# Kernel optimization log

Measured on AMD Instinct MI355X. Metric: run time of the kernel, lower is better.

The kernel has to match this reference:

```python
import jax, jax.numpy as jnp
import numpy as np
import math

H = 16
D = 1024
DH = D // H  # 64


def setup_inputs() -> dict:
    key = jax.random.key(0)
    ks = jax.random.split(key, 11)
    B, N = 2, 2048
    f = lambda k, shape, s=1.0: jax.random.normal(k, shape, dtype=jnp.float32) * s
    return {
        "x_q": f(ks[0], (B, N, D)),
        "x_k": f(ks[1], (B, N, D)),
        "x_v": f(ks[2], (B, N, D)),
        "Wq": f(ks[3], (D, D), 0.02),
        "bq": f(ks[4], (D,), 0.02),
        "Wk": f(ks[5], (D, D), 0.02),
        "bk": f(ks[6], (D,), 0.02),
        "Wv": f(ks[7], (D, D), 0.02),
        "bv": f(ks[8], (D,), 0.02),
        "Wo": f(ks[9], (D, D), 0.02),
        "bo": f(ks[10], (D,), 0.02),
    }


def _mha(x_q, x_k, x_v, Wq, bq, Wk, bk, Wv, bv, Wo, bo):
    B, N, _ = x_q.shape
    # torch nn.Linear: y = x @ W.T + b
    def proj(x, W, b):
        y = x @ W.T + b                      # [B, N, D]
        return y.reshape(B, N, H, DH).transpose(0, 2, 1, 3)  # [B, H, N, DH]
    Q = proj(x_q, Wq, bq)
    K = proj(x_k, Wk, bk)
    V = proj(x_v, Wv, bv)
    scores = jnp.einsum("bhqd,bhkd->bhqk", Q, K) / math.sqrt(DH)  # [B,H,N,N]
    attn = jax.nn.softmax(scores, axis=-1)
    X = jnp.einsum("bhqk,bhkd->bhqd", attn, V)   # [B,H,N,DH]
    X = X.transpose(0, 2, 1, 3).reshape(B, N, D)  # concat heads
    return X @ Wo.T + bo


def reference(x_q, x_k, x_v, Wq, bq, Wk, bk, Wv, bv, Wo, bo):
    return _mha(x_q, x_k, x_v, Wq, bq, Wk, bk, Wv, bv, Wo, bo)
```

## Files before the change

### kernel.cpp

```cpp
#include <hip/hip_runtime.h>

typedef unsigned short u16;
typedef __attribute__((ext_vector_type(8))) short s16x8;
typedef __attribute__((ext_vector_type(4))) float f32x4;

#define B_  2
#define N_  2048
#define D_  1024
#define H_  16
#define DH_ 64
#define M_  4096

#define S_X (M_ * D_)
#define S_W (D_ * D_)

#define QSCALE 0.1803368801111204f

#define OFF_QB 0
#define OFF_KB (S_X)
#define OFF_VB (2 * S_X)
#define OFF_XB (3 * S_X)
#define OFF_XQ (4 * S_X)
#define OFF_XK (5 * S_X)
#define OFF_XV (6 * S_X)
#define OFF_WQ (7 * S_X)
#define OFF_WK (7 * S_X + S_W)
#define OFF_WV (7 * S_X + 2 * S_W)
#define OFF_WO (7 * S_X + 3 * S_W)
#define WS_FAST_BYTES ((size_t)(7 * S_X + 4 * S_W) * 2)

#if __has_builtin(__builtin_amdgcn_exp2f)
#define EXP2(x) __builtin_amdgcn_exp2f(x)
#else
#define EXP2(x) exp2f(x)
#endif

__device__ __forceinline__ u16 f2bf(float f) {
  unsigned u = __builtin_bit_cast(unsigned, f);
  u += 0x7fffu + ((u >> 16) & 1u);
  return (u16)(u >> 16);
}
__device__ __forceinline__ s16x8 pack8(float4 a, float4 b) {
  s16x8 r;
  r[0] = (short)f2bf(a.x); r[1] = (short)f2bf(a.y);
  r[2] = (short)f2bf(a.z); r[3] = (short)f2bf(a.w);
  r[4] = (short)f2bf(b.x); r[5] = (short)f2bf(b.y);
  r[6] = (short)f2bf(b.z); r[7] = (short)f2bf(b.w);
  return r;
}
__device__ __forceinline__ void gl2lds16(const void* g, void* l) {
  __builtin_amdgcn_global_load_lds(
      (const __attribute__((address_space(1))) void*)g,
      (__attribute__((address_space(3))) void*)l, 16, 0, 0);
}

__global__ __launch_bounds__(256)
void cvt_kernel(const float* __restrict__ p0, const float* __restrict__ p1,
                const float* __restrict__ p2, const float* __restrict__ p3,
                const float* __restrict__ p4, const float* __restrict__ p5,
                const float* __restrict__ p6, u16* __restrict__ ws) {
  const float* src; u16* dst; int n;
  switch (blockIdx.y) {
    case 0:  src = p0; dst = ws + OFF_XQ; n = S_X; break;
    case 1:  src = p1; dst = ws + OFF_XK; n = S_X; break;
    case 2:  src = p2; dst = ws + OFF_XV; n = S_X; break;
    case 3:  src = p3; dst = ws + OFF_WQ; n = S_W; break;
    case 4:  src = p4; dst = ws + OFF_WK; n = S_W; break;
    case 5:  src = p5; dst = ws + OFF_WV; n = S_W; break;
    default: src = p6; dst = ws + OFF_WO; n = S_W; break;
  }
  const int stride = gridDim.x * blockDim.x * 4;
  for (int idx = (blockIdx.x * blockDim.x + threadIdx.x) * 4; idx < n; idx += stride) {
    const float4 v = *(const float4*)&src[idx];
    ushort4 o;
    o.x = f2bf(v.x); o.y = f2bf(v.y); o.z = f2bf(v.z); o.w = f2bf(v.w);
    *(ushort4*)&dst[idx] = o;
  }
}

__global__ __launch_bounds__(256, 3)
void qkv_gemm_bf(const u16* __restrict__ ws_in, const float* __restrict__ bq,
                 const float* __restrict__ bk, const float* __restrict__ bv,
                 u16* __restrict__ ws_out) {
  __shared__ __align__(16) u16 As[128 * 32];
  __shared__ __align__(16) u16 Bs[128 * 32];
  const int flat = (blockIdx.z * 32 + blockIdx.y) * 8 + blockIdx.x;
  const int u = flat & 7, v = flat >> 3;
  const int bxn = v & 7;
  const int byz = u * 12 + (v >> 3);
  const int z = byz >> 5, bym = byz & 31;

  const u16* A = ws_in + OFF_XQ + (size_t)z * S_X;
  const u16* W = ws_in + OFF_WQ + (size_t)z * S_W;
  const float* bias = (z == 0) ? bq : (z == 1) ? bk : bv;
  u16* out = ws_out + (size_t)z * S_X;
  const float scale = (z == 0) ? QSCALE : 1.0f;

  const int tid  = threadIdx.x;
  const int wave = tid >> 6, lane = tid & 63;
  const int quad = lane >> 4, l16 = lane & 15;
  const int wr = wave >> 1, wc = wave & 1;
  const int m0 = bym * 128, n0 = bxn * 128;

  f32x4 acc[4][4];
#pragma unroll
  for (int i = 0; i < 4; ++i)
#pragma unroll
    for (int j = 0; j < 4; ++j) acc[i][j] = {0.f, 0.f, 0.f, 0.f};

  for (int kt = 0; kt < D_ / 32; ++kt) {
    const int kb = kt * 32;
#pragma unroll
    for (int call = 0; call < 2; ++call) {
      const int c = call * 256 + wave * 64 + lane;
      const int row = c >> 2, col8 = (c & 3) * 8;
      gl2lds16(&A[(size_t)(m0 + row) * D_ + kb + col8],
               &As[(size_t)(call * 256 + wave * 64) * 8]);
      gl2lds16(&W[(size_t)(n0 + row) * D_ + kb + col8],
               &Bs[(size_t)(call * 256 + wave * 64) * 8]);
    }
    __syncthreads();

    s16x8 af[4], bf[4];
#pragma unroll
    for (int i = 0; i < 4; ++i) {
      af[i] = *(const s16x8*)&As[(wr * 64 + i * 16 + l16) * 32 + quad * 8];
      bf[i] = *(const s16x8*)&Bs[(wc * 64 + i * 16 + l16) * 32 + quad * 8];
    }
#pragma unroll
    for (int i = 0; i < 4; ++i)
#pragma unroll
      for (int j = 0; j < 4; ++j)
        acc[i][j] = __builtin_amdgcn_mfma_f32_16x16x32_bf16(af[i], bf[j], acc[i][j], 0, 0, 0);
    __syncthreads();
  }

  if (z != 2) {
#pragma unroll
    for (int j = 0; j < 4; ++j) {
      const int col = n0 + wc * 64 + j * 16 + l16;
      const float bvv = bias[col];
#pragma unroll
      for (int i = 0; i < 4; ++i) {
        const int row0 = m0 + wr * 64 + i * 16 + quad * 4;
#pragma unroll
        for (int r = 0; r < 4; ++r)
          out[(size_t)(row0 + r) * D_ + col] = f2bf((acc[i][j][r] + bvv) * scale);
      }
    }
  } else {
#pragma unroll
    for (int j = 0; j < 4; ++j) {
      const int col = n0 + wc * 64 + j * 16 + l16;
      const int h = col >> 6, dh = col & 63;
      const float bvv = bias[col];
#pragma unroll
      for (int i = 0; i < 4; ++i) {
        const int row0 = m0 + wr * 64 + i * 16 + quad * 4;
#pragma unroll
        for (int r = 0; r < 4; ++r) {
          const int tok = row0 + r;
          const int b = tok >> 11, t = tok & (N_ - 1);
          out[(size_t)((b * H_ + h) * DH_ + dh) * N_ + t] = f2bf(acc[i][j][r] + bvv);
        }
      }
    }
  }
}

__global__ __launch_bounds__(256, 3)
void qkv_gemm_f32(const float* __restrict__ xq, const float* __restrict__ xk,
                  const float* __restrict__ xv, const float* __restrict__ Wq,
                  const float* __restrict__ Wk, const float* __restrict__ Wv,
                  const float* __restrict__ bq, const float* __restrict__ bk,
                  const float* __restrict__ bv, u16* __restrict__ ws) {
  __shared__ __align__(16) u16 As[128 * 32];
  __shared__ __align__(16) u16 Bs[128 * 32];
  const int flat = (blockIdx.z * 32 + blockIdx.y) * 8 + blockIdx.x;
  const int u = flat & 7, v = flat >> 3;
  const int bxn = v & 7;
  const int byz = u * 12 + (v >> 3);
  const int z = byz >> 5, bym = byz & 31;

  const float* A    = (z == 0) ? xq : (z == 1) ? xk : xv;
  const float* W    = (z == 0) ? Wq : (z == 1) ? Wk : Wv;
  const float* bias = (z == 0) ? bq : (z == 1) ? bk : bv;
  u16* out = ws + (size_t)z * S_X;
  const float scale = (z == 0) ? QSCALE : 1.0f;

  const int tid  = threadIdx.x;
  const int wave = tid >> 6, lane = tid & 63;
  const int quad = lane >> 4, l16 = lane & 15;
  const int wr = wave >> 1, wc = wave & 1;
  const int m0 = bym * 128, n0 = bxn * 128;

  f32x4 acc[4][4];
#pragma unroll
  for (int i = 0; i < 4; ++i)
#pragma unroll
    for (int j = 0; j < 4; ++j) acc[i][j] = {0.f, 0.f, 0.f, 0.f};

  for (int kt = 0; kt < D_ / 32; ++kt) {
    const int kb = kt * 32;
#pragma unroll
    for (int call = 0; call < 2; ++call) {
      const int c = call * 256 + wave * 64 + lane;
      const int row = c >> 2, col = (c & 3) * 8;
      const float4 a0 = *(const float4*)&A[(size_t)(m0 + row) * D_ + kb + col];
      const float4 a1 = *(const float4*)&A[(size_t)(m0 + row) * D_ + kb + col + 4];
      const float4 w0 = *(const float4*)&W[(size_t)(n0 + row) * D_ + kb + col];
      const float4 w1 = *(const float4*)&W[(size_t)(n0 + row) * D_ + kb + col + 4];
      *(s16x8*)&As[c * 8] = pack8(a0, a1);
      *(s16x8*)&Bs[c * 8] = pack8(w0, w1);
    }
    __syncthreads();

    s16x8 af[4], bf[4];
#pragma unroll
    for (int i = 0; i < 4; ++i) {
      af[i] = *(const s16x8*)&As[(wr * 64 + i * 16 + l16) * 32 + quad * 8];
      bf[i] = *(const s16x8*)&Bs[(wc * 64 + i * 16 + l16) * 32 + quad * 8];
    }
#pragma unroll
    for (int i = 0; i < 4; ++i)
#pragma unroll
      for (int j = 0; j < 4; ++j)
        acc[i][j] = __builtin_amdgcn_mfma_f32_16x16x32_bf16(af[i], bf[j], acc[i][j], 0, 0, 0);
    __syncthreads();
  }

  if (z != 2) {
#pragma unroll
    for (int j = 0; j < 4; ++j) {
      const int col = n0 + wc * 64 + j * 16 + l16;
      const float bvv = bias[col];
#pragma unroll
      for (int i = 0; i < 4; ++i) {
        const int row0 = m0 + wr * 64 + i * 16 + quad * 4;
#pragma unroll
        for (int r = 0; r < 4; ++r)
          out[(size_t)(row0 + r) * D_ + col] = f2bf((acc[i][j][r] + bvv) * scale);
      }
    }
  } else {
#pragma unroll
    for (int j = 0; j < 4; ++j) {
      const int col = n0 + wc * 64 + j * 16 + l16;
      const int h = col >> 6, dh = col & 63;
      const float bvv = bias[col];
#pragma unroll
      for (int i = 0; i < 4; ++i) {
        const int row0 = m0 + wr * 64 + i * 16 + quad * 4;
#pragma unroll
        for (int r = 0; r < 4; ++r) {
          const int tok = row0 + r;
          const int b = tok >> 11, t = tok & (N_ - 1);
          out[(size_t)((b * H_ + h) * DH_ + dh) * N_ + t] = f2bf(acc[i][j][r] + bvv);
        }
      }
    }
  }
}

__global__ __launch_bounds__(256, 2)
void attn_kernel(const u16* __restrict__ Q, const u16* __restrict__ K,
                 const u16* __restrict__ Vt, u16* __restrict__ X) {
  __shared__ __align__(16) u16 Ks[128 * 64];
  __shared__ __align__(16) u16 Vs[64 * 128];
  const int tid  = threadIdx.x;
  const int wave = tid >> 6, lane = tid & 63;
  const int quad = lane >> 4, l16 = lane & 15;

  const int flat = blockIdx.y * 16 + blockIdx.x;
  const int u = flat & 7, slot = flat >> 3;
  const int qb = slot & 15;
  const int bh = u * 4 + (slot >> 4);
  const int q0 = qb * 128;
  const int b = bh >> 4, h = bh & 15;

  s16x8 qfa[2], qfb[2];
#pragma unroll
  for (int ks = 0; ks < 2; ++ks) {
    qfa[ks] = *(const s16x8*)&Q[(size_t)(b * N_ + q0 + wave * 16 + l16) * D_ +
                                h * 64 + ks * 32 + quad * 8];
    qfb[ks] = *(const s16x8*)&Q[(size_t)(b * N_ + q0 + 64 + wave * 16 + l16) * D_ +
                                h * 64 + ks * 32 + quad * 8];
  }

  f32x4 oa[4], ob[4];
#pragma unroll
  for (int mt = 0; mt < 4; ++mt) { oa[mt] = {0.f, 0.f, 0.f, 0.f}; ob[mt] = {0.f, 0.f, 0.f, 0.f}; }
  float lia = 0.f, lib = 0.f;

  for (int kt = 0; kt < N_ / 128; ++kt) {
    const int k0 = kt * 128;
#pragma unroll
    for (int c4 = 0; c4 < 4; ++c4) {
      const int p = c4 * 256 + wave * 64 + lane;
      { const int row = p >> 3, cd = p & 7, src = cd ^ (row & 7);
        gl2lds16(&K[(size_t)(b * N_ + k0 + row) * D_ + h * 64 + src * 8],
                 &Ks[(size_t)(c4 * 256 + wave * 64) * 8]); }
      { const int row = p >> 4, cd = p & 15;
        const int src = (cd & 8) | ((cd & 7) ^ (row & 7));
        gl2lds16(&Vt[(size_t)((b * H_ + h) * DH_ + row) * N_ + k0 + src * 8],
                 &Vs[(size_t)(c4 * 256 + wave * 64) * 8]); }
    }
    __syncthreads();

    f32x4 sa[8], sb[8];
#pragma unroll
    for (int nt = 0; nt < 8; ++nt) { sa[nt] = {0.f, 0.f, 0.f, 0.f}; sb[nt] = {0.f, 0.f, 0.f, 0.f}; }
    __builtin_amdgcn_s_setprio(1);
#pragma unroll
    for (int nt = 0; nt < 8; ++nt) {
      const int row = nt * 16 + l16;
      const s16x8 kf0 = *(const s16x8*)&Ks[row * 64 + ((quad    ) ^ (l16 & 7)) * 8];
      const s16x8 kf1 = *(const s16x8*)&Ks[row * 64 + ((4 + quad) ^ (l16 & 7)) * 8];
      sa[nt] = __builtin_amdgcn_mfma_f32_16x16x32_bf16(kf0, qfa[0], sa[nt], 0, 0, 0);
      sa[nt] = __builtin_amdgcn_mfma_f32_16x16x32_bf16(kf1, qfa[1], sa[nt], 0, 0, 0);
      sb[nt] = __builtin_amdgcn_mfma_f32_16x16x32_bf16(kf0, qfb[0], sb[nt], 0, 0, 0);
      sb[nt] = __builtin_amdgcn_mfma_f32_16x16x32_bf16(kf1, qfb[1], sb[nt], 0, 0, 0);
    }
    __builtin_amdgcn_s_setprio(0);

    unsigned pka[8][2], pkb[8][2];
    float psa = 0.f, psb = 0.f;
#pragma unroll
    for (int nt = 0; nt < 8; ++nt) {
      { const unsigned b0 = __builtin_bit_cast(unsigned, EXP2(sa[nt][0]));
        const unsigned b1 = __builtin_bit_cast(unsigned, EXP2(sa[nt][1]));
        const unsigned b2 = __builtin_bit_cast(unsigned, EXP2(sa[nt][2]));
        const unsigned b3 = __builtin_bit_cast(unsigned, EXP2(sa[nt][3]));
        pka[nt][0] = (b0 >> 16) | (b1 & 0xffff0000u);
        pka[nt][1] = (b2 >> 16) | (b3 & 0xffff0000u);
        psa += __builtin_bit_cast(float, b0 & 0xffff0000u);
        psa += __builtin_bit_cast(float, b1 & 0xffff0000u);
        psa += __builtin_bit_cast(float, b2 & 0xffff0000u);
        psa += __builtin_bit_cast(float, b3 & 0xffff0000u); }
      { const unsigned b0 = __builtin_bit_cast(unsigned, EXP2(sb[nt][0]));
        const unsigned b1 = __builtin_bit_cast(unsigned, EXP2(sb[nt][1]));
        const unsigned b2 = __builtin_bit_cast(unsigned, EXP2(sb[nt][2]));
        const unsigned b3 = __builtin_bit_cast(unsigned, EXP2(sb[nt][3]));
        pkb[nt][0] = (b0 >> 16) | (b1 & 0xffff0000u);
        pkb[nt][1] = (b2 >> 16) | (b3 & 0xffff0000u);
        psb += __builtin_bit_cast(float, b0 & 0xffff0000u);
        psb += __builtin_bit_cast(float, b1 & 0xffff0000u);
        psb += __builtin_bit_cast(float, b2 & 0xffff0000u);
        psb += __builtin_bit_cast(float, b3 & 0xffff0000u); }
    }
    lia += psa; lib += psb;

#pragma unroll
    for (int k2 = 0; k2 < 4; ++k2) {
      s16x8 vf[4];
#pragma unroll
      for (int mt = 0; mt < 4; ++mt) {
        const int row = mt * 16 + l16;
        const int j8 = k2 * 4 + quad;
        const int cd = (j8 & 8) | ((j8 & 7) ^ (row & 7));
        vf[mt] = *(const s16x8*)&Vs[row * 128 + cd * 8];
      }
      int bda[4], bdb[4];
#pragma unroll
      for (int d = 0; d < 4; ++d) {
        const int sc = ((quad & 1) * 2 + (d >> 1)) * 16 + l16;
        { const int ve = __shfl((int)pka[k2 * 2][d & 1], sc);
          const int vo = __shfl((int)pka[k2 * 2 + 1][d & 1], sc);
          bda[d] = (quad >> 1) ? vo : ve; }
        { const int ve = __shfl((int)pkb[k2 * 2][d & 1], sc);
          const int vo = __shfl((int)pkb[k2 * 2 + 1][d & 1], sc);
          bdb[d] = (quad >> 1) ? vo : ve; }
      }
      const s16x8 bfa = __builtin_bit_cast(s16x8, *(int4*)bda);
      const s16x8 bfb = __builtin_bit_cast(s16x8, *(int4*)bdb);
      __builtin_amdgcn_s_setprio(1);
#pragma unroll
      for (int mt = 0; mt < 4; ++mt) {
        oa[mt] = __builtin_amdgcn_mfma_f32_16x16x32_bf16(vf[mt], bfa, oa[mt], 0, 0, 0);
        ob[mt] = __builtin_amdgcn_mfma_f32_16x16x32_bf16(vf[mt], bfb, ob[mt], 0, 0, 0);
      }
      __builtin_amdgcn_s_setprio(0);
    }
    __syncthreads();
  }

  lia += __shfl_xor(lia, 16);
  lia += __shfl_xor(lia, 32);
  lib += __shfl_xor(lib, 16);
  lib += __shfl_xor(lib, 32);
  const float inva = 1.0f / lia;
  const float invb = 1.0f / lib;
  const int qa = q0 + wave * 16 + l16;
#pragma unroll
  for (int mt = 0; mt < 4; ++mt) {
    ushort4 w;
    w.x = f2bf(oa[mt][0] * inva);
    w.y = f2bf(oa[mt][1] * inva);
    w.z = f2bf(oa[mt][2] * inva);
    w.w = f2bf(oa[mt][3] * inva);
    *(ushort4*)&X[(size_t)(b * N_ + qa) * D_ + h * 64 + mt * 16 + quad * 4] = w;
  }
#pragma unroll
  for (int mt = 0; mt < 4; ++mt) {
    ushort4 w;
    w.x = f2bf(ob[mt][0] * invb);
    w.y = f2bf(ob[mt][1] * invb);
    w.z = f2bf(ob[mt][2] * invb);
    w.w = f2bf(ob[mt][3] * invb);
    *(ushort4*)&X[(size_t)(b * N_ + qa + 64) * D_ + h * 64 + mt * 16 + quad * 4] = w;
  }
}

__global__ __launch_bounds__(256, 2)
void out_gemm_bf(const u16* __restrict__ A, const u16* __restrict__ W,
                 const float* __restrict__ bias, float* __restrict__ out) {
  __shared__ __align__(16) u16 As[64 * 32];
  __shared__ __align__(16) u16 Bs[128 * 32];
  const int tid  = threadIdx.x;
  const int wave = tid >> 6, lane = tid & 63;
  const int quad = lane >> 4, l16 = lane & 15;
  const int wr = wave >> 1, wc = wave & 1;

  const int flat = blockIdx.y * 8 + blockIdx.x;
  const int u = flat & 7, v = flat >> 3;
  const int bxn = v & 7;
  const int bym = u * 8 + (v >> 3);
  const int m0 = bym * 64, n0 = bxn * 128;

  f32x4 acc[2][4];
#pragma unroll
  for (int i = 0; i < 2; ++i)
#pragma unroll
    for (int j = 0; j < 4; ++j) acc[i][j] = {0.f, 0.f, 0.f, 0.f};

  for (int kt = 0; kt < D_ / 32; ++kt) {
    const int kb = kt * 32;
    { const int c = wave * 64 + lane;
      const int row = c >> 2, col8 = (c & 3) * 8;
      gl2lds16(&A[(size_t)(m0 + row) * D_ + kb + col8], &As[(size_t)(wave * 64) * 8]); }
#pragma unroll
    for (int call = 0; call < 2; ++call) {
      const int c = call * 256 + wave * 64 + lane;
      const int row = c >> 2, col8 = (c & 3) * 8;
      gl2lds16(&W[(size_t)(n0 + row) * D_ + kb + col8],
               &Bs[(size_t)(call * 256 + wave * 64) * 8]);
    }
    __syncthreads();

    s16x8 af[2], bf[4];
#pragma unroll
    for (int i = 0; i < 2; ++i)
      af[i] = *(const s16x8*)&As[(wr * 32 + i * 16 + l16) * 32 + quad * 8];
#pragma unroll
    for (int j = 0; j < 4; ++j)
      bf[j] = *(const s16x8*)&Bs[(wc * 64 + j * 16 + l16) * 32 + quad * 8];
#pragma unroll
    for (int i = 0; i < 2; ++i)
#pragma unroll
      for (int j = 0; j < 4; ++j)
        acc[i][j] = __builtin_amdgcn_mfma_f32_16x16x32_bf16(af[i], bf[j], acc[i][j], 0, 0, 0);
    __syncthreads();
  }

#pragma unroll
  for (int j = 0; j < 4; ++j) {
    const int col = n0 + wc * 64 + j * 16 + l16;
    const float bv = bias[col];
#pragma unroll
    for (int i = 0; i < 2; ++i) {
      const int row0 = m0 + wr * 32 + i * 16 + quad * 4;
#pragma unroll
      for (int r = 0; r < 4; ++r)
        out[(size_t)(row0 + r) * D_ + col] = acc[i][j][r] + bv;
    }
  }
}

__global__ __launch_bounds__(256, 2)
void out_gemm_f32(const u16* __restrict__ A, const float* __restrict__ W,
                  const float* __restrict__ bias, float* __restrict__ out) {
  __shared__ __align__(16) u16 As[64 * 32];
  __shared__ __align__(16) u16 Bs[128 * 32];
  const int tid  = threadIdx.x;
  const int wave = tid >> 6, lane = tid & 63;
  const int quad = lane >> 4, l16 = lane & 15;
  const int wr = wave >> 1, wc = wave & 1;

  const int flat = blockIdx.y * 8 + blockIdx.x;
  const int u = flat & 7, v = flat >> 3;
  const int bxn = v & 7;
  const int bym = u * 8 + (v >> 3);
  const int m0 = bym * 64, n0 = bxn * 128;

  f32x4 acc[2][4];
#pragma unroll
  for (int i = 0; i < 2; ++i)
#pragma unroll
    for (int j = 0; j < 4; ++j) acc[i][j] = {0.f, 0.f, 0.f, 0.f};

  for (int kt = 0; kt < D_ / 32; ++kt) {
    const int kb = kt * 32;
    { const int c = wave * 64 + lane;
      const int row = c >> 2, col = (c & 3) * 8;
      gl2lds16(&A[(size_t)(m0 + row) * D_ + kb + col], &As[(size_t)(wave * 64) * 8]); }
#pragma unroll
    for (int call = 0; call < 2; ++call) {
      const int c = call * 256 + wave * 64 + lane;
      const int row = c >> 2, col = (c & 3) * 8;
      const float4 w0 = *(const float4*)&W[(size_t)(n0 + row) * D_ + kb + col];
      const float4 w1 = *(const float4*)&W[(size_t)(n0 + row) * D_ + kb + col + 4];
      *(s16x8*)&Bs[c * 8] = pack8(w0, w1);
    }
    __syncthreads();

    s16x8 af[2], bf[4];
#pragma unroll
    for (int i = 0; i < 2; ++i)
      af[i] = *(const s16x8*)&As[(wr * 32 + i * 16 + l16) * 32 + quad * 8];
#pragma unroll
    for (int j = 0; j < 4; ++j)
      bf[j] = *(const s16x8*)&Bs[(wc * 64 + j * 16 + l16) * 32 + quad * 8];
#pragma unroll
    for (int i = 0; i < 2; ++i)
#pragma unroll
      for (int j = 0; j < 4; ++j)
        acc[i][j] = __builtin_amdgcn_mfma_f32_16x16x32_bf16(af[i], bf[j], acc[i][j], 0, 0, 0);
    __syncthreads();
  }

#pragma unroll
  for (int j = 0; j < 4; ++j) {
    const int col = n0 + wc * 64 + j * 16 + l16;
    const float bv = bias[col];
#pragma unroll
    for (int i = 0; i < 2; ++i) {
      const int row0 = m0 + wr * 32 + i * 16 + quad * 4;
#pragma unroll
      for (int r = 0; r < 4; ++r)
        out[(size_t)(row0 + r) * D_ + col] = acc[i][j][r] + bv;
    }
  }
}

extern "C" void kernel_launch(void* const* d_in, const int* in_sizes, int n_in,
                              void* d_out, int out_size, void* d_ws, size_t ws_size,
                              hipStream_t stream) {
  const float* xq = (const float*)d_in[0];
  const float* xk = (const float*)d_in[1];
  const float* xv = (const float*)d_in[2];
  const float* Wq = (const float*)d_in[3];
  const float* bq = (const float*)d_in[4];
  const float* Wk = (const float*)d_in[5];
  const float* bk = (const float*)d_in[6];
  const float* Wv = (const float*)d_in[7];
  const float* bv = (const float*)d_in[8];
  const float* Wo = (const float*)d_in[9];
  const float* bo = (const float*)d_in[10];
  u16*   ws  = (u16*)d_ws;
  float* out = (float*)d_out;

  dim3 blk(256);
  if (ws_size >= WS_FAST_BYTES) {
    hipLaunchKernelGGL(cvt_kernel, dim3(256, 7), blk, 0, stream,
                       xq, xk, xv, Wq, Wk, Wv, Wo, ws);
    hipLaunchKernelGGL(qkv_gemm_bf, dim3(8, 32, 3), blk, 0, stream,
                       ws, bq, bk, bv, ws + OFF_QB);
    hipLaunchKernelGGL(attn_kernel, dim3(16, 32), blk, 0, stream,
                       ws + OFF_QB, ws + OFF_KB, ws + OFF_VB, ws + OFF_XB);
    hipLaunchKernelGGL(out_gemm_bf, dim3(8, 64), blk, 0, stream,
                       ws + OFF_XB, ws + OFF_WO, bo, out);
  } else {
    hipLaunchKernelGGL(qkv_gemm_f32, dim3(8, 32, 3), blk, 0, stream,
                       xq, xk, xv, Wq, Wk, Wv, bq, bk, bv, ws);
    hipLaunchKernelGGL(attn_kernel, dim3(16, 32), blk, 0, stream,
                       ws + OFF_QB, ws + OFF_KB, ws + OFF_VB, ws + OFF_XB);
    hipLaunchKernelGGL(out_gemm_f32, dim3(8, 64), blk, 0, stream,
                       ws + OFF_XB, Wo, bo, out);
  }
}
```

Before: 229.9 us.

## Double-buffer K/V tiles in attention kernel to overlap loads with MFMA

Attention kernel now keeps two LDS buffers for K and V tiles and issues the direct global-to-LDS loads for the next key tile before computing on the current one. Explicit vmcnt waits and barriers replace the __syncthreads pairs, so memory latency can hide behind the QK and PV matrix math. LDS use per block doubles to 64KB, which with two blocks per CU may limit occupancy. The correctness of the vmcnt(8) count depends on each stage issuing exactly 8 loads.

```diff
diff --git a/kernel.cpp b/kernel.cpp
--- a/kernel.cpp
+++ b/kernel.cpp
@@ -265,8 +265,8 @@
 __global__ __launch_bounds__(256, 2)
 void attn_kernel(const u16* __restrict__ Q, const u16* __restrict__ K,
                  const u16* __restrict__ Vt, u16* __restrict__ X) {
-  __shared__ __align__(16) u16 Ks[128 * 64];
-  __shared__ __align__(16) u16 Vs[64 * 128];
+  __shared__ __align__(16) u16 Ks[2][128 * 64];
+  __shared__ __align__(16) u16 Vs[2][64 * 128];
   const int tid  = threadIdx.x;
   const int wave = tid >> 6, lane = tid & 63;
   const int quad = lane >> 4, l16 = lane & 15;
@@ -292,20 +292,36 @@
   for (int mt = 0; mt < 4; ++mt) { oa[mt] = {0.f, 0.f, 0.f, 0.f}; ob[mt] = {0.f, 0.f, 0.f, 0.f}; }
   float lia = 0.f, lib = 0.f;
 
-  for (int kt = 0; kt < N_ / 128; ++kt) {
+  auto stage = [&](int buf, int kt) {
     const int k0 = kt * 128;
 #pragma unroll
     for (int c4 = 0; c4 < 4; ++c4) {
       const int p = c4 * 256 + wave * 64 + lane;
       { const int row = p >> 3, cd = p & 7, src = cd ^ (row & 7);
         gl2lds16(&K[(size_t)(b * N_ + k0 + row) * D_ + h * 64 + src * 8],
-                 &Ks[(size_t)(c4 * 256 + wave * 64) * 8]); }
+                 &Ks[buf][(size_t)(c4 * 256 + wave * 64) * 8]); }
       { const int row = p >> 4, cd = p & 15;
         const int src = (cd & 8) | ((cd & 7) ^ (row & 7));
         gl2lds16(&Vt[(size_t)((b * H_ + h) * DH_ + row) * N_ + k0 + src * 8],
-                 &Vs[(size_t)(c4 * 256 + wave * 64) * 8]); }
-    }
-    __syncthreads();
+                 &Vs[buf][(size_t)(c4 * 256 + wave * 64) * 8]); }
+    }
+  };
+
+  stage(0, 0);
+  int cur = 0;
+
+  for (int kt = 0; kt < N_ / 128; ++kt) {
+    if (kt + 1 < N_ / 128) {
+      stage(cur ^ 1, kt + 1);
+      asm volatile("s_waitcnt vmcnt(8)" ::: "memory");
+    } else {
+      asm volatile("s_waitcnt vmcnt(0)" ::: "memory");
+    }
+    __builtin_amdgcn_sched_barrier(0);
+    __builtin_amdgcn_s_barrier();
+
+    const u16* ks = &Ks[cur][0];
+    const u16* vs = &Vs[cur][0];
 
     f32x4 sa[8], sb[8];
 #pragma unroll
@@ -314,8 +330,8 @@
 #pragma unroll
     for (int nt = 0; nt < 8; ++nt) {
       const int row = nt * 16 + l16;
-      const s16x8 kf0 = *(const s16x8*)&Ks[row * 64 + ((quad    ) ^ (l16 & 7)) * 8];
-      const s16x8 kf1 = *(const s16x8*)&Ks[row * 64 + ((4 + quad) ^ (l16 & 7)) * 8];
+      const s16x8 kf0 = *(const s16x8*)&ks[row * 64 + ((quad    ) ^ (l16 & 7)) * 8];
+      const s16x8 kf1 = *(const s16x8*)&ks[row * 64 + ((4 + quad) ^ (l16 & 7)) * 8];
       sa[nt] = __builtin_amdgcn_mfma_f32_16x16x32_bf16(kf0, qfa[0], sa[nt], 0, 0, 0);
       sa[nt] = __builtin_amdgcn_mfma_f32_16x16x32_bf16(kf1, qfa[1], sa[nt], 0, 0, 0);
       sb[nt] = __builtin_amdgcn_mfma_f32_16x16x32_bf16(kf0, qfb[0], sb[nt], 0, 0, 0);
@@ -358,7 +374,7 @@
         const int row = mt * 16 + l16;
         const int j8 = k2 * 4 + quad;
         const int cd = (j8 & 8) | ((j8 & 7) ^ (row & 7));
-        vf[mt] = *(const s16x8*)&Vs[row * 128 + cd * 8];
+        vf[mt] = *(const s16x8*)&vs[row * 128 + cd * 8];
       }
       int bda[4], bdb[4];
 #pragma unroll
@@ -381,7 +397,10 @@
       }
       __builtin_amdgcn_s_setprio(0);
     }
-    __syncthreads();
+
+    asm volatile("s_waitcnt lgkmcnt(0)" ::: "memory");
+    __builtin_amdgcn_s_barrier();
+    cur ^= 1;
   }
 
   lia += __shfl_xor(lia, 16);
```

Result: no change. 230.3 us (+0.2%).
